# Kernel tuning notes

Measured on AMD Instinct MI355X. Metric: run time of the kernel, lower is better.

Reference implementation:

```python
import jax, jax.numpy as jnp
import numpy as np

TOP_K = 8
SCALE = 2.5  # routed_scaling_factor


def setup_inputs() -> dict:
    key = jax.random.key(0)
    k1, k2, k3 = jax.random.split(key, 3)
    x = jax.random.normal(k1, (4, 4096, 4096), dtype=jnp.float32)
    weight = jax.random.normal(k2, (256, 4096), dtype=jnp.float32) * 0.02  # [n_experts, hidden]
    bias = jax.random.normal(k3, (256,), dtype=jnp.float32) * 0.01  # e_score_correction_bias
    return {"x": x, "weight": weight, "bias": bias}


def reference(x, weight, bias):
    # x: [B, S, H] -> flatten to tokens
    t = x.reshape(-1, x.shape[-1])                      # [T, H]
    logits = jnp.einsum('th,eh->te', t, weight)         # gate linear, [T, E]
    scores = jax.nn.sigmoid(logits)
    scores_for_choice = scores + bias[None, :]          # bias-corrected scores
    topk_weight, topk_idx = jax.lax.top_k(scores_for_choice, TOP_K)  # [T, K]
    denom = jnp.sum(topk_weight, axis=-1, keepdims=True) + 1e-20
    topk_weight = (topk_weight / denom) * SCALE
    return topk_idx, topk_weight
```

## Files before the change

kernel.cpp:

```cpp
#include <hip/hip_runtime.h>
#include <hip/hip_bf16.h>
#include <math.h>


using f16x8  = __attribute__((ext_vector_type(8))) _Float16;
using f32x16 = __attribute__((ext_vector_type(16))) float;

constexpr int E_EXPERTS = 256;
constexpr int KDIM      = 4096;
constexpr int TOPK      = 8;
constexpr float SCALE   = 2.5f;

constexpr int BM = 64, BN = 128, BK = 64, NT = 256;
constexpr int NSTEP = KDIM / BK;
constexpr float F16_MIN_NORMAL = 6.1035156e-5f;

__device__ __forceinline__ void load_lds16(const short* g, short* l) {
    auto gp = (const __attribute__((address_space(1))) short*)g;
    auto lp = (__attribute__((address_space(3))) short*)(uintptr_t)l;
    __builtin_amdgcn_global_load_lds(gp, lp, 16, 0, 0);
}

__global__ void wsplit_kernel(const float* __restrict__ W, short* __restrict__ W1,
                              short* __restrict__ W2) {
    int i = blockIdx.x * 256 + threadIdx.x;
    float4 w = ((const float4*)W)[i];
    float v[4] = {w.x, w.y, w.z, w.w};
    short o1[4], o2[4];
#pragma unroll
    for (int j = 0; j < 4; ++j) {
        _Float16 h1 = (fabsf(v[j]) >= F16_MIN_NORMAL) ? (_Float16)v[j] : (_Float16)0.0f;
        _Float16 h2 = (_Float16)((v[j] - (float)h1) * 4096.0f);
        o1[j] = __builtin_bit_cast(short, h1);
        o2[j] = __builtin_bit_cast(short, h2);
    }
    ((short4*)W1)[i] = make_short4(o1[0], o1[1], o1[2], o1[3]);
    ((short4*)W2)[i] = make_short4(o2[0], o2[1], o2[2], o2[3]);
}

__global__ __launch_bounds__(NT, 2) void gate_gemm(
    const float* __restrict__ X,
    const short* __restrict__ W1, const short* __restrict__ W2,
    const float* __restrict__ Bias, float* __restrict__ S) {
    __shared__ short lds[32768];

    const int tid  = threadIdx.x;
    const int lane = tid & 63;
    const int w    = tid >> 6;
    const int wm   = w >> 1;
    const int wn   = w & 1;

    const int p       = blockIdx.x;
    const int cpx     = gridDim.x >> 3;
    const int logical = (p & 7) * cpx + (p >> 3);
    const int tok0 = (logical >> 1) * BM;
    const int e0   = (logical & 1) * BN;

    const float* xa = X + (size_t)(tok0 + wm * 32 + (lane & 31)) * KDIM + (lane >> 5) * 8;

    int bsrc[4], bdst[4];
#pragma unroll
    for (int j = 0; j < 4; ++j) {
        int f = j * 256 + tid;
        int e = f >> 3, pc = f & 7;
        int c = pc ^ (e & 7);
        bsrc[j] = (e0 + e) * KDIM + c * 8;
        bdst[j] = f * 8;
    }

    int bro[2][4];
#pragma unroll
    for (int nt = 0; nt < 2; ++nt) {
        int e = wn * 64 + nt * 32 + (lane & 31);
#pragma unroll
        for (int ks4 = 0; ks4 < 4; ++ks4) {
            int pc = (ks4 * 2 + (lane >> 5)) ^ (e & 7);
            bro[nt][ks4] = e * 64 + pc * 8;
        }
    }

    auto stage = [&](int bufOff, int k0) {
#pragma unroll
        for (int j = 0; j < 4; ++j) {
            load_lds16(W1 + (size_t)bsrc[j] + k0, &lds[bufOff + bdst[j]]);
            load_lds16(W2 + (size_t)bsrc[j] + k0, &lds[bufOff + 8192 + bdst[j]]);
        }
    };

    float4 raw[4][2];
    auto loadA = [&](int ks) {
#pragma unroll
        for (int ks4 = 0; ks4 < 4; ++ks4) {
            const float* s = xa + (size_t)ks * BK + ks4 * 16;
            raw[ks4][0] = *(const float4*)s;
            raw[ks4][1] = *(const float4*)(s + 4);
        }
    };

    f32x16 accM[2], accC[2];
#pragma unroll
    for (int nt = 0; nt < 2; ++nt)
#pragma unroll
        for (int j = 0; j < 16; ++j) { accM[nt][j] = 0.0f; accC[nt][j] = 0.0f; }

    stage(0, 0);
    loadA(0);

    int buf = 0;
    for (int ks = 0; ks < NSTEP; ++ks) {
        __syncthreads();

        if (ks + 1 < NSTEP) stage((buf ^ 1) * 16384, (ks + 1) * BK);

        f16x8 fa1[4], fa2[4];
#pragma unroll
        for (int ks4 = 0; ks4 < 4; ++ks4) {
            float v[8] = {raw[ks4][0].x, raw[ks4][0].y, raw[ks4][0].z, raw[ks4][0].w,
                          raw[ks4][1].x, raw[ks4][1].y, raw[ks4][1].z, raw[ks4][1].w};
#pragma unroll
            for (int j = 0; j < 8; ++j) {
                _Float16 h1 = (fabsf(v[j]) >= F16_MIN_NORMAL) ? (_Float16)v[j] : (_Float16)0.0f;
                _Float16 h2 = (_Float16)((v[j] - (float)h1) * 4096.0f);
                fa1[ks4][j] = h1;
                fa2[ks4][j] = h2;
            }
        }

        if (ks + 1 < NSTEP) loadA(ks + 1);

        const int bo = buf * 16384;
#pragma unroll
        for (int nt = 0; nt < 2; ++nt) {
            f16x8 b1[4], b2[4];
#pragma unroll
            for (int ks4 = 0; ks4 < 4; ++ks4) {
                b1[ks4] = *(const f16x8*)&lds[bo + bro[nt][ks4]];
                b2[ks4] = *(const f16x8*)&lds[bo + 8192 + bro[nt][ks4]];
            }
            f32x16 cM = accM[nt], cC = accC[nt];
#pragma unroll
            for (int ks4 = 0; ks4 < 4; ++ks4) {
                cM = __builtin_amdgcn_mfma_f32_32x32x16_f16(fa1[ks4], b1[ks4], cM, 0, 0, 0);
                cC = __builtin_amdgcn_mfma_f32_32x32x16_f16(fa1[ks4], b2[ks4], cC, 0, 0, 0);
                cC = __builtin_amdgcn_mfma_f32_32x32x16_f16(fa2[ks4], b1[ks4], cC, 0, 0, 0);
            }
            accM[nt] = cM;
            accC[nt] = cC;
        }
        buf ^= 1;
    }

#pragma unroll
    for (int nt = 0; nt < 2; ++nt) {
        const int ec = e0 + wn * 64 + nt * 32 + (lane & 31);
        const float bv = Bias[ec];
#pragma unroll
        for (int reg = 0; reg < 16; ++reg) {
            const int tr = tok0 + wm * 32 + (reg & 3) + 8 * (reg >> 2) + 4 * (lane >> 5);
            const float logit = accM[nt][reg] + accC[nt][reg] * (1.0f / 4096.0f);
            S[(size_t)tr * E_EXPERTS + ec] = 1.0f / (1.0f + expf(-logit)) + bv;
        }
    }
}

__global__ __launch_bounds__(256) void gate_topk(
    const float* __restrict__ S, float* __restrict__ outIdx,
    float* __restrict__ outW, int T) {
    const int wave = threadIdx.x >> 6;
    const int lane = threadIdx.x & 63;
    const int t    = blockIdx.x * 4 + wave;
    if (t >= T) return;

    const float* row = S + (size_t)t * E_EXPERTS;
    float v[4];
    int   idx[4];
#pragma unroll
    for (int j = 0; j < 4; ++j) {
        idx[j] = lane + 64 * j;
        v[j]   = row[idx[j]];
    }

    float tv[TOPK];
    int   ti[TOPK];
#pragma unroll
    for (int k = 0; k < TOPK; ++k) {
        float bv = v[0];
        int   bi = idx[0];
#pragma unroll
        for (int j = 1; j < 4; ++j)
            if (v[j] > bv) { bv = v[j]; bi = idx[j]; }
#pragma unroll
        for (int off = 1; off < 64; off <<= 1) {
            float ov = __shfl_xor(bv, off);
            int   oi = __shfl_xor(bi, off);
            if (ov > bv || (ov == bv && oi < bi)) { bv = ov; bi = oi; }
        }
        tv[k] = bv;
        ti[k] = bi;
#pragma unroll
        for (int j = 0; j < 4; ++j)
            if (idx[j] == bi) v[j] = -INFINITY;
    }

    float denom = 0.0f;
#pragma unroll
    for (int k = 0; k < TOPK; ++k) denom += tv[k];
    denom += 1e-20f;

#pragma unroll
    for (int k = 0; k < TOPK; ++k) {
        if (lane == k) {
            outIdx[(size_t)t * TOPK + k] = (float)ti[k];
            outW[(size_t)t * TOPK + k]   = (tv[k] / denom) * SCALE;
        }
    }
}

extern "C" void kernel_launch(void* const* d_in, const int* in_sizes, int n_in,
                              void* d_out, int out_size, void* d_ws, size_t ws_size,
                              hipStream_t stream) {
    const float* x    = (const float*)d_in[0];
    const float* w    = (const float*)d_in[1];
    const float* bias = (const float*)d_in[2];

    const int T = in_sizes[0] / KDIM;

    float* S  = (float*)d_ws;
    short* W1 = (short*)((char*)d_ws + (size_t)T * E_EXPERTS * 4);
    short* W2 = W1 + (size_t)E_EXPERTS * KDIM;

    float* outIdx = (float*)d_out;
    float* outW   = outIdx + (size_t)T * TOPK;

    wsplit_kernel<<<(E_EXPERTS * KDIM / 4) / 256, 256, 0, stream>>>(w, W1, W2);
    gate_gemm<<<(T / BM) * (E_EXPERTS / BN), NT, 0, stream>>>(x, W1, W2, bias, S);
    gate_topk<<<T / 4, 256, 0, stream>>>(S, outIdx, outW, T);
}
```

Before: 217.6 us.

## Double waves per GEMM block, each wave computing one 32x32 tile

```diff
diff --git a/kernel.cpp b/kernel.cpp
--- a/kernel.cpp
+++ b/kernel.cpp
@@ -11,7 +11,7 @@
 constexpr int TOPK      = 8;
 constexpr float SCALE   = 2.5f;
 
-constexpr int BM = 64, BN = 128, BK = 64, NT = 256;
+constexpr int BM = 64, BN = 128, BK = 64, NT = 512;
 constexpr int NSTEP = KDIM / BK;
 constexpr float F16_MIN_NORMAL = 6.1035156e-5f;
 
@@ -38,7 +38,7 @@
     ((short4*)W2)[i] = make_short4(o2[0], o2[1], o2[2], o2[3]);
 }
 
-__global__ __launch_bounds__(NT, 2) void gate_gemm(
+__global__ __launch_bounds__(NT, 4) void gate_gemm(
     const float* __restrict__ X,
     const short* __restrict__ W1, const short* __restrict__ W2,
     const float* __restrict__ Bias, float* __restrict__ S) {
@@ -47,8 +47,8 @@
     const int tid  = threadIdx.x;
     const int lane = tid & 63;
     const int w    = tid >> 6;
-    const int wm   = w >> 1;
-    const int wn   = w & 1;
+    const int wm   = w >> 2;
+    const int wn   = w & 3;
 
     const int p       = blockIdx.x;
     const int cpx     = gridDim.x >> 3;
@@ -58,30 +58,29 @@
 
     const float* xa = X + (size_t)(tok0 + wm * 32 + (lane & 31)) * KDIM + (lane >> 5) * 8;
 
-    int bsrc[4], bdst[4];
-#pragma unroll
-    for (int j = 0; j < 4; ++j) {
-        int f = j * 256 + tid;
+    int bsrc[2], bdst[2];
+#pragma unroll
+    for (int j = 0; j < 2; ++j) {
+        int f = j * 512 + tid;
         int e = f >> 3, pc = f & 7;
         int c = pc ^ (e & 7);
         bsrc[j] = (e0 + e) * KDIM + c * 8;
         bdst[j] = f * 8;
     }
 
-    int bro[2][4];
-#pragma unroll
-    for (int nt = 0; nt < 2; ++nt) {
-        int e = wn * 64 + nt * 32 + (lane & 31);
+    int bro[4];
+    {
+        int e = wn * 32 + (lane & 31);
 #pragma unroll
         for (int ks4 = 0; ks4 < 4; ++ks4) {
             int pc = (ks4 * 2 + (lane >> 5)) ^ (e & 7);
-            bro[nt][ks4] = e * 64 + pc * 8;
+            bro[ks4] = e * 64 + pc * 8;
         }
     }
 
     auto stage = [&](int bufOff, int k0) {
 #pragma unroll
-        for (int j = 0; j < 4; ++j) {
+        for (int j = 0; j < 2; ++j) {
             load_lds16(W1 + (size_t)bsrc[j] + k0, &lds[bufOff + bdst[j]]);
             load_lds16(W2 + (size_t)bsrc[j] + k0, &lds[bufOff + 8192 + bdst[j]]);
         }
@@ -97,11 +96,9 @@
         }
     };
 
-    f32x16 accM[2], accC[2];
-#pragma unroll
-    for (int nt = 0; nt < 2; ++nt)
-#pragma unroll
-        for (int j = 0; j < 16; ++j) { accM[nt][j] = 0.0f; accC[nt][j] = 0.0f; }
+    f32x16 accM, accC;
+#pragma unroll
+    for (int j = 0; j < 16; ++j) { accM[j] = 0.0f; accC[j] = 0.0f; }
 
     stage(0, 0);
     loadA(0);
@@ -129,35 +126,28 @@
         if (ks + 1 < NSTEP) loadA(ks + 1);
 
         const int bo = buf * 16384;
-#pragma unroll
-        for (int nt = 0; nt < 2; ++nt) {
-            f16x8 b1[4], b2[4];
-#pragma unroll
-            for (int ks4 = 0; ks4 < 4; ++ks4) {
-                b1[ks4] = *(const f16x8*)&lds[bo + bro[nt][ks4]];
-                b2[ks4] = *(const f16x8*)&lds[bo + 8192 + bro[nt][ks4]];
-            }
-            f32x16 cM = accM[nt], cC = accC[nt];
-#pragma unroll
-            for (int ks4 = 0; ks4 < 4; ++ks4) {
-                cM = __builtin_amdgcn_mfma_f32_32x32x16_f16(fa1[ks4], b1[ks4], cM, 0, 0, 0);
-                cC = __builtin_amdgcn_mfma_f32_32x32x16_f16(fa1[ks4], b2[ks4], cC, 0, 0, 0);
-                cC = __builtin_amdgcn_mfma_f32_32x32x16_f16(fa2[ks4], b1[ks4], cC, 0, 0, 0);
-            }
-            accM[nt] = cM;
-            accC[nt] = cC;
+        f16x8 b1[4], b2[4];
+#pragma unroll
+        for (int ks4 = 0; ks4 < 4; ++ks4) {
+            b1[ks4] = *(const f16x8*)&lds[bo + bro[ks4]];
+            b2[ks4] = *(const f16x8*)&lds[bo + 8192 + bro[ks4]];
+        }
+#pragma unroll
+        for (int ks4 = 0; ks4 < 4; ++ks4) {
+            accM = __builtin_amdgcn_mfma_f32_32x32x16_f16(fa1[ks4], b1[ks4], accM, 0, 0, 0);
+            accC = __builtin_amdgcn_mfma_f32_32x32x16_f16(fa1[ks4], b2[ks4], accC, 0, 0, 0);
+            accC = __builtin_amdgcn_mfma_f32_32x32x16_f16(fa2[ks4], b1[ks4], accC, 0, 0, 0);
         }
         buf ^= 1;
     }
 
-#pragma unroll
-    for (int nt = 0; nt < 2; ++nt) {
-        const int ec = e0 + wn * 64 + nt * 32 + (lane & 31);
+    {
+        const int ec = e0 + wn * 32 + (lane & 31);
         const float bv = Bias[ec];
 #pragma unroll
         for (int reg = 0; reg < 16; ++reg) {
             const int tr = tok0 + wm * 32 + (reg & 3) + 8 * (reg >> 2) + 4 * (lane >> 5);
-            const float logit = accM[nt][reg] + accC[nt][reg] * (1.0f / 4096.0f);
+            const float logit = accM[reg] + accC[reg] * (1.0f / 4096.0f);
             S[(size_t)tr * E_EXPERTS + ec] = 1.0f / (1.0f + expf(-logit)) + bv;
         }
     }
```

Result: slower. 325.9 us (+49.8%).
